# Kernel optimization log

Hardware: AMD Instinct MI355X
Metric: run time of the kernel (lower is better)

Reference implementation:

```python
import jax, jax.numpy as jnp
import numpy as np

# --- constants mirroring init_kwargs ---
DIM = 1024
N_HEADS = 16
N_KV_HEADS = 4
HEAD_DIM = DIM // N_HEADS          # 64
REP = N_HEADS // N_KV_HEADS        # 4
ROPE_THETA = 10000.0
WINDOW = 512
N_GLOBAL = 64
EPS = 1e-6


def setup_inputs() -> dict:
    key = jax.random.key(0)
    ks = jax.random.split(key, 7)
    B, L = 2, 2048
    x = jax.random.normal(ks[0], (B, L, DIM), dtype=jnp.float32)
    s = 0.02
    wq = jax.random.normal(ks[1], (DIM, N_HEADS * HEAD_DIM), dtype=jnp.float32) * s
    wk = jax.random.normal(ks[2], (DIM, N_KV_HEADS * HEAD_DIM), dtype=jnp.float32) * s
    wv = jax.random.normal(ks[3], (DIM, N_KV_HEADS * HEAD_DIM), dtype=jnp.float32) * s
    wo = jax.random.normal(ks[4], (N_HEADS * HEAD_DIM, DIM), dtype=jnp.float32) * s
    gq = jnp.ones((HEAD_DIM,), dtype=jnp.float32) + 0.01 * jax.random.normal(ks[5], (HEAD_DIM,), dtype=jnp.float32)
    gk = jnp.ones((HEAD_DIM,), dtype=jnp.float32) + 0.01 * jax.random.normal(ks[6], (HEAD_DIM,), dtype=jnp.float32)
    return {"x": x, "wq": wq, "wk": wk, "wv": wv, "wo": wo, "gq": gq, "gk": gk}


def _rmsnorm(t, g):
    # QKNorm: RMS norm over head_dim with learnable per-dim scale
    return t * jax.lax.rsqrt(jnp.mean(t * t, axis=-1, keepdims=True) + EPS) * g


def _rope(t, cos, sin):
    # t: [B,H,L,hd]; complex RoPE over consecutive pairs (2i, 2i+1)
    t1 = t[..., 0::2]
    t2 = t[..., 1::2]
    o1 = t1 * cos - t2 * sin
    o2 = t1 * sin + t2 * cos
    return jnp.stack([o1, o2], axis=-1).reshape(t.shape)


def reference(x, wq, wk, wv, wo, gq, gk):
    B, L, D = x.shape
    q = (x @ wq).reshape(B, L, N_HEADS, HEAD_DIM)
    k = (x @ wk).reshape(B, L, N_KV_HEADS, HEAD_DIM)
    v = (x @ wv).reshape(B, L, N_KV_HEADS, HEAD_DIM)
    q = _rmsnorm(q, gq)
    k = _rmsnorm(k, gk)
    q = q.transpose(0, 2, 1, 3)  # [B,H,L,hd]
    k = k.transpose(0, 2, 1, 3)
    v = v.transpose(0, 2, 1, 3)

    # RoPE frequencies (start_pos = 0)
    inv_freq = 1.0 / (ROPE_THETA ** (jnp.arange(0, HEAD_DIM, 2, dtype=jnp.float32) / HEAD_DIM))
    ang = jnp.arange(L, dtype=jnp.float32)[:, None] * inv_freq[None, :]  # [L, hd/2]
    cos, sin = jnp.cos(ang), jnp.sin(ang)
    q = _rope(q, cos, sin)
    k = _rope(k, cos, sin)

    # GQA: repeat kv heads (repeat_interleave on head dim)
    k = jnp.repeat(k, REP, axis=1)
    v = jnp.repeat(v, REP, axis=1)

    scores = jnp.einsum("bhqd,bhkd->bhqk", q, k) / np.sqrt(HEAD_DIM).astype(np.float32)

    # sliding-window + global-token causal mask
    half = WINDOW // 2
    i = jnp.arange(L)[:, None]
    j = jnp.arange(L)[None, :]
    m = (j <= i) & ((j >= i - half) | (j < N_GLOBAL))  # [L,L] bool
    scores = jnp.where(m[None, None], scores, -jnp.inf)

    attn = jax.nn.softmax(scores.astype(jnp.float32), axis=-1).astype(scores.dtype)
    out = jnp.einsum("bhqk,bhkd->bhqd", attn, v)
    out = out.transpose(0, 2, 1, 3).reshape(B, L, N_HEADS * HEAD_DIM)
    return out @ wo
```

## Files before the change

kernel.cpp:

```cpp
#include <hip/hip_runtime.h>
#include <hip/hip_bf16.h>

typedef __bf16 bf16x8 __attribute__((ext_vector_type(8)));
typedef __bf16 bf16x4 __attribute__((ext_vector_type(4)));
typedef float  f32x4  __attribute__((ext_vector_type(4)));
typedef short  s16x4  __attribute__((ext_vector_type(4)));

__device__ __forceinline__ __bf16 to_bf16(float f) {
    __hip_bfloat16 h = __float2bfloat16(f);
    return *reinterpret_cast<__bf16*>(&h);
}

__device__ __forceinline__ f32x4 mfma32(bf16x8 a, bf16x8 b, f32x4 c) {
    return __builtin_amdgcn_mfma_f32_16x16x32_bf16(a, b, c, 0, 0, 0);
}
__device__ __forceinline__ f32x4 mfma16(bf16x4 a, bf16x4 b, f32x4 c) {
#if __has_builtin(__builtin_amdgcn_mfma_f32_16x16x16_bf16)
    return __builtin_amdgcn_mfma_f32_16x16x16_bf16(a, b, c, 0, 0, 0);
#else
    return __builtin_amdgcn_mfma_f32_16x16x16bf16_1k(
        __builtin_bit_cast(s16x4, a), __builtin_bit_cast(s16x4, b), c, 0, 0, 0);
#endif
}

__device__ __forceinline__ void gload_lds16(const __bf16* g, __bf16* l) {
    __builtin_amdgcn_global_load_lds(
        (const __attribute__((address_space(1))) void*)g,
        (__attribute__((address_space(3))) void*)l, 16, 0, 0);
}


__global__ __launch_bounds__(256) void prep_k(const float* __restrict__ wq,
                                              const float* __restrict__ wk,
                                              const float* __restrict__ wv,
                                              const float* __restrict__ x,
                                              __bf16* __restrict__ WqkvT,
                                              __bf16* __restrict__ xb,
                                              float2* __restrict__ rope_tab) {
    int b = blockIdx.x, tid = threadIdx.x;
    if (b >= 3584) {
        int idx = (b - 3584) * 256 + tid;
        int pos = idx >> 5, f = idx & 31;
        float ex = (float)(2 * f) * (1.0f / 64.0f);
        float invf = expf(-ex * 9.210340371976184f);
        float ang = (float)pos * invf;
        rope_tab[idx] = make_float2(cosf(ang), sinf(ang));
        return;
    }
    if (b >= 1536) {
        int i = ((b - 1536) * 256 + tid) * 8;
        f32x4 a = *(const f32x4*)(x + i);
        f32x4 c = *(const f32x4*)(x + i + 4);
        bf16x8 h;
        h[0] = to_bf16(a.x); h[1] = to_bf16(a.y); h[2] = to_bf16(a.z); h[3] = to_bf16(a.w);
        h[4] = to_bf16(c.x); h[5] = to_bf16(c.y); h[6] = to_bf16(c.z); h[7] = to_bf16(c.w);
        *(bf16x8*)(xb + i) = h;
        return;
    }
    __shared__ float tile[32][33];
    const float* src; __bf16* dst; int N, idx;
    if (b < 1024)      { src = wq; dst = WqkvT;                        N = 1024; idx = b; }
    else if (b < 1280) { src = wk; dst = WqkvT + (size_t)1024 * 1024;  N = 256;  idx = b - 1024; }
    else               { src = wv; dst = WqkvT + (size_t)1280 * 1024;  N = 256;  idx = b - 1280; }
    int k0 = (idx & 31) * 32, n0 = (idx >> 5) * 32;
    int tx = tid & 31, ty = tid >> 5;
#pragma unroll
    for (int r = 0; r < 4; ++r) {
        int kk = ty + r * 8;
        tile[kk][tx] = src[(size_t)(k0 + kk) * N + n0 + tx];
    }
    __syncthreads();
#pragma unroll
    for (int r = 0; r < 4; ++r) {
        int nn = ty + r * 8;
        dst[(size_t)(n0 + nn) * 1024 + k0 + tx] = to_bf16(tile[tx][nn]);
    }
}

#define GEMM_CORE128(A, BT, K, M0, N0)                                          \
    __bf16* smem = (__bf16*)smem_raw;                                           \
    int tid = threadIdx.x;                                                      \
    int m0 = (M0), n0 = (N0);                                                   \
    int wid = tid >> 6, lane = tid & 63;                                        \
    int wm = (wid & 1) * 64, wn = (wid >> 1) * 32;                              \
    int lm = lane & 15, qd = lane >> 4;                                         \
    int srow = tid >> 2, sc4 = tid & 3;                                         \
    f32x4 acc[4][2] = {};                                                       \
    int nt = (K) / 64;                                                          \
    auto STAGE = [&](int bsel, int t) {                                         \
        __bf16* base = smem + bsel * 16384;                                     \
        _Pragma("unroll")                                                       \
        for (int kh = 0; kh < 2; ++kh)                                          \
            gload_lds16((A) + (size_t)(m0 + srow) * (K) + t * 64 + kh * 32 + sc4 * 8, \
                        base + kh * 4096 + wid * 512);                          \
        _Pragma("unroll")                                                       \
        for (int kh = 0; kh < 2; ++kh)                                          \
            gload_lds16((BT) + (size_t)(n0 + srow) * (K) + t * 64 + kh * 32 + sc4 * 8, \
                        base + 8192 + kh * 4096 + wid * 512);                   \
    };                                                                          \
    STAGE(0, 0);                                                                \
    for (int t = 0; t < nt; ++t) {                                              \
        if (t + 1 < nt) {                                                       \
            STAGE((t + 1) & 1, t + 1);                                          \
            asm volatile("s_waitcnt vmcnt(4)" ::: "memory");                    \
        } else {                                                                \
            asm volatile("s_waitcnt vmcnt(0)" ::: "memory");                    \
        }                                                                       \
        __builtin_amdgcn_s_barrier();                                           \
        __builtin_amdgcn_sched_barrier(0);                                      \
        const __bf16* cA = smem + (t & 1) * 16384;                              \
        const __bf16* cB = cA + 8192;                                           \
        _Pragma("unroll")                                                       \
        for (int kh = 0; kh < 2; ++kh) {                                        \
            bf16x8 af[4], bfr[2];                                               \
            _Pragma("unroll")                                                   \
            for (int t4 = 0; t4 < 4; ++t4) {                                    \
                int row = wm + t4 * 16 + lm;                                    \
                af[t4] = *(const bf16x8*)&cA[kh * 4096 + row * 32 + qd * 8];    \
            }                                                                   \
            _Pragma("unroll")                                                   \
            for (int j = 0; j < 2; ++j) {                                       \
                int col = wn + j * 16 + lm;                                     \
                bfr[j] = *(const bf16x8*)&cB[kh * 4096 + col * 32 + qd * 8];    \
            }                                                                   \
            _Pragma("unroll")                                                   \
            for (int ti = 0; ti < 4; ++ti)                                      \
                _Pragma("unroll")                                               \
                for (int tj = 0; tj < 2; ++tj)                                  \
                    acc[ti][tj] = mfma32(af[ti], bfr[tj], acc[ti][tj]);         \
        }                                                                       \
        asm volatile("s_waitcnt lgkmcnt(0)" ::: "memory");                      \
        __builtin_amdgcn_s_barrier();                                           \
    }

__global__ __launch_bounds__(512) void gemmqkv_k(const __bf16* __restrict__ A,
                                                 const __bf16* __restrict__ BT,
                                                 const float2* __restrict__ rope_tab,
                                                 const float* __restrict__ gq,
                                                 const float* __restrict__ gk,
                                                 const float* __restrict__ wo,
                                                 __bf16* __restrict__ Qb,
                                                 __bf16* __restrict__ Kbl,
                                                 __bf16* __restrict__ Vt,
                                                 __bf16* __restrict__ WoT) {
    extern __shared__ char smem_raw[];
    if (blockIdx.y >= 12) {
        float* scr = (float*)smem_raw;
        int bidT = (blockIdx.y - 12) * 32 + blockIdx.x;
        int sub = threadIdx.x >> 8, t8 = threadIdx.x & 255;
        int tx = t8 & 31, ty = t8 >> 5;
        float* my = scr + sub * 1056;
#pragma unroll
        for (int r = 0; r < 4; ++r) {
            int tile = bidT * 8 + r * 2 + sub;
            int k0 = (tile & 31) * 32, n0t = (tile >> 5) * 32;
            __syncthreads();
#pragma unroll
            for (int rr = 0; rr < 4; ++rr) {
                int kk = ty + rr * 8;
                my[kk * 33 + tx] = wo[(size_t)(k0 + kk) * 1024 + n0t + tx];
            }
            __syncthreads();
#pragma unroll
            for (int rr = 0; rr < 4; ++rr) {
                int nn = ty + rr * 8;
                WoT[(size_t)(n0t + nn) * 1024 + k0 + tx] = to_bf16(my[tx * 33 + nn]);
            }
        }
        return;
    }
    __shared__ float ssp[4][128];
    int gidb = blockIdx.y * 32 + blockIdx.x;
    int swzb = (gidb & 7) * 48 + (gidb >> 3);
    GEMM_CORE128(A, BT, 1024, (swzb & 31) * 128, (swzb >> 5) * 128)
    int head0 = n0 >> 6;
    int quad = wid >> 1;
    int chead = wn & 63;

    if (head0 < 20) {
        int head = head0 + (quad >> 1);
        bool isq = head < 16;
        const float* gvec = isq ? gq : gk;
        float gam[2];
#pragma unroll
        for (int tj = 0; tj < 2; ++tj) gam[tj] = gvec[chead + tj * 16 + lm];

#pragma unroll
        for (int ti = 0; ti < 4; ++ti)
#pragma unroll
            for (int r = 0; r < 4; ++r) {
                float sq = acc[ti][0][r] * acc[ti][0][r] + acc[ti][1][r] * acc[ti][1][r];
                sq += __shfl_xor(sq, 1);
                sq += __shfl_xor(sq, 2);
                sq += __shfl_xor(sq, 4);
                sq += __shfl_xor(sq, 8);
                if (lm == 0) ssp[quad][wm + ti * 16 + qd * 4 + r] = sq;
            }
        __syncthreads();

#pragma unroll
        for (int ti = 0; ti < 4; ++ti)
#pragma unroll
            for (int r = 0; r < 4; ++r) {
                int row = wm + ti * 16 + qd * 4 + r;
                int t = m0 + row;
                int pos = t & 2047, bb = t >> 11;
                float ss = ssp[quad][row] + ssp[quad ^ 1][row];
                float scale = rsqrtf(ss * (1.0f / 64.0f) + 1e-6f);
#pragma unroll
                for (int tj = 0; tj < 2; ++tj) {
                    int cw = chead + tj * 16 + lm;
                    float v = acc[ti][tj][r] * scale * gam[tj];
                    float2 cs = rope_tab[pos * 32 + (cw >> 1)];
                    float pv = __shfl_xor(v, 1);
                    float outv = (cw & 1) ? (pv * cs.y + v * cs.x) : (v * cs.x - pv * cs.y);
                    if (isq) {
                        int kvh = head >> 2, h4 = head & 3;
                        size_t off = (((((size_t)bb * 4 + kvh) * 128 + (pos >> 4)) * 4 + h4) * 16
                                      + (pos & 15)) * 64 + cw;
                        Qb[off] = to_bf16(outv * 0.125f);
                    } else {
                        int kvg = head - 16;
                        Kbl[(((size_t)bb * 4 + kvg) * 2048 + pos) * 64 + cw] = to_bf16(outv);
                    }
                }
            }
    } else {
        __bf16* tvh = smem + (quad >> 1) * 8704;
        int bb = m0 >> 11, pos0 = m0 & 2047;
#pragma unroll
        for (int ti = 0; ti < 4; ++ti)
#pragma unroll
            for (int tj = 0; tj < 2; ++tj)
#pragma unroll
                for (int r = 0; r < 4; ++r) {
                    int row = wm + ti * 16 + qd * 4 + r;
                    int cw = chead + tj * 16 + lm;
                    tvh[cw * 136 + row] = to_bf16(acc[ti][tj][r]);
                }
        __syncthreads();
        int hh = tid >> 8, t8 = tid & 255;
        int kvg = head0 + hh - 20;
        size_t gg = (size_t)bb * 4 + kvg;
        const __bf16* tvr = smem + hh * 8704;
#pragma unroll
        for (int p = 0; p < 4; ++p) {
            int d = p * 16 + (t8 >> 4);
            int tok = (t8 & 15) * 8;
            bf16x8 vvv = *(const bf16x8*)&tvr[d * 136 + tok];
            *(bf16x8*)(Vt + (gg * 64 + d) * 2048 + pos0 + tok) = vvv;
        }
    }
}

__global__ __launch_bounds__(512) void gemm_bf16_k(const __bf16* __restrict__ A,
                                                   const __bf16* __restrict__ BT,
                                                   float* __restrict__ C,
                                                   int K, int N) {
    extern __shared__ char smem_raw[];
    int gidb = blockIdx.y * 32 + blockIdx.x;
    int swzb = (gidb & 7) * 32 + (gidb >> 3);
    GEMM_CORE128(A, BT, K, (swzb & 31) * 128, (swzb >> 5) * 128)
#pragma unroll
    for (int ti = 0; ti < 4; ++ti)
#pragma unroll
        for (int tj = 0; tj < 2; ++tj)
#pragma unroll
            for (int r = 0; r < 4; ++r) {
                int row = m0 + wm + ti * 16 + qd * 4 + r;
                int col = n0 + wn + tj * 16 + lm;
                C[(size_t)row * N + col] = acc[ti][tj][r];
            }
}

__global__ __launch_bounds__(512) void attn_k(const __bf16* __restrict__ Qb,
                                              const __bf16* __restrict__ Kbl,
                                              const __bf16* __restrict__ Vt,
                                              __bf16* __restrict__ aout) {
    __shared__ __bf16 Kt[2][64 * 64];
    __shared__ __bf16 Vl[2][64 * 64];
    int tid = threadIdx.x, wid = tid >> 6, lane = tid & 63;
    int l15 = lane & 15, quad = lane >> 4;
    int qb = blockIdx.x, kvh = blockIdx.y, b = blockIdx.z;
    int qg = wid >> 2;
    int h4 = wid & 3;
    int iw0 = qb * 32;
    int iw = iw0 + qg * 16;
    int g = b * 4 + kvh;
    int h = kvh * 4 + h4;
    int e7 = l15 & 7;

    int qbi = qb * 2 + qg;
    const __bf16* qp = Qb + ((((size_t)g * 128 + qbi) * 4 + h4) * 16 + l15) * 64 + quad * 8;
    bf16x8 qf0 = *(const bf16x8*)qp;
    bf16x8 qf1 = *(const bf16x8*)(qp + 32);

    int ts = (iw0 - 256) >> 6; if (ts < 1) ts = 1;
    int tmaxb = (iw0 + 31) >> 6;
    int n_all = (tmaxb >= ts) ? (tmaxb - ts + 2) : 1;
    int tmaxw = (iw + 15) >> 6;

    const __bf16* Kg = Kbl + (size_t)g * 2048 * 64;
    const __bf16* Vg = Vt + (size_t)g * 64 * 2048;

    int r0 = tid >> 3, c0 = tid & 7;
    int kl = r0 * 64 + ((c0 ^ (r0 & 7)) * 8);

    bf16x8 kr, vr;
    auto stage_load = [&](int tt) {
        kr = *(const bf16x8*)(Kg + (size_t)tt * 64 * 64 + r0 * 64 + c0 * 8);
        vr = *(const bf16x8*)(Vg + (size_t)r0 * 2048 + tt * 64 + c0 * 8);
    };
    auto stage_write = [&](int buf) {
        *(bf16x8*)&Kt[buf][kl] = kr;
        *(bf16x8*)&Vl[buf][kl] = vr;
    };

    stage_load(0);
    stage_write(0);

    f32x4 o[4] = {};
    float mr = -1e30f, lrp = 0.f;
    int iq = iw + l15;

    for (int idx = 0; idx < n_all; ++idx) {
        int tt = (idx == 0) ? 0 : ts + idx - 1;
        if (idx + 1 < n_all) stage_load(ts + idx);
        __syncthreads();
        int buf = idx & 1;

        f32x4 s[4] = {};
#pragma unroll
        for (int nt = 0; nt < 4; ++nt) {
            const __bf16* kp = &Kt[buf][(nt * 16 + l15) * 64];
            bf16x8 k0 = *(const bf16x8*)(kp + ((quad ^ e7) * 8));
            bf16x8 k1 = *(const bf16x8*)(kp + (((quad + 4) ^ e7) * 8));
            s[nt] = mfma32(k0, qf0, s[nt]);
            s[nt] = mfma32(k1, qf1, s[nt]);
        }

        bool need_mask = (tt >= tmaxw) || (tt >= 1 && tt * 64 < iw + 15 - 256);
        if (need_mask) {
#pragma unroll
            for (int nt = 0; nt < 4; ++nt)
#pragma unroll
                for (int r = 0; r < 4; ++r) {
                    int j = tt * 64 + nt * 16 + quad * 4 + r;
                    bool valid = (j <= iq) && ((j >= iq - 256) || (j < 64));
                    s[nt][r] = valid ? s[nt][r] : -1e30f;
                }
        }

        float mx = -1e30f;
#pragma unroll
        for (int nt = 0; nt < 4; ++nt)
#pragma unroll
            for (int r = 0; r < 4; ++r) mx = fmaxf(mx, s[nt][r]);
        mx = fmaxf(mx, __shfl_xor(mx, 16));
        mx = fmaxf(mx, __shfl_xor(mx, 32));
        float mn = fmaxf(mr, mx);
        float alpha = __expf(mr - mn);
        mr = mn;

        float ps = 0.f;
        bf16x4 pb[4];
#pragma unroll
        for (int nt = 0; nt < 4; ++nt)
#pragma unroll
            for (int r = 0; r < 4; ++r) {
                float pv = __expf(s[nt][r] - mn);
                ps += pv;
                pb[nt][r] = to_bf16(pv);
            }
        lrp = lrp * alpha + ps;

#pragma unroll
        for (int dt = 0; dt < 4; ++dt) {
            o[dt] *= alpha;
            const __bf16* vp = &Vl[buf][(dt * 16 + l15) * 64];
#pragma unroll
            for (int nt = 0; nt < 4; ++nt) {
                int c8 = 2 * nt + (quad >> 1);
                bf16x4 va = *(const bf16x4*)(vp + ((c8 ^ e7) * 8) + (quad & 1) * 4);
                o[dt] = mfma16(va, pb[nt], o[dt]);
            }
        }

        if (idx + 1 < n_all) stage_write((idx + 1) & 1);
    }

    lrp += __shfl_xor(lrp, 16);
    lrp += __shfl_xor(lrp, 32);
    float inv = 1.f / lrp;
    __syncthreads();
    __bf16* pr = (__bf16*)Kt + wid * 16 * 64;
#pragma unroll
    for (int dt = 0; dt < 4; ++dt)
#pragma unroll
        for (int r = 0; r < 4; ++r) {
            int e = dt * 16 + quad * 4 + r;
            int c8 = e >> 3;
            pr[l15 * 64 + ((c8 ^ e7) * 8) + (e & 7)] = to_bf16(o[dt][r] * inv);
        }
    bf16x8 o0 = *(const bf16x8*)(pr + l15 * 64 + (((2 * quad) ^ e7) * 8));
    bf16x8 o1 = *(const bf16x8*)(pr + l15 * 64 + (((2 * quad + 1) ^ e7) * 8));
    __bf16* op = aout + ((size_t)b * 2048 + iw + l15) * 1024 + h * 64 + quad * 16;
    *(bf16x8*)op = o0;
    *(bf16x8*)(op + 8) = o1;
}

extern "C" void kernel_launch(void* const* d_in, const int* in_sizes, int n_in,
                              void* d_out, int out_size, void* d_ws, size_t ws_size,
                              hipStream_t stream) {
    const float* x  = (const float*)d_in[0];
    const float* wq = (const float*)d_in[1];
    const float* wk = (const float*)d_in[2];
    const float* wv = (const float*)d_in[3];
    const float* wo = (const float*)d_in[4];
    const float* gq = (const float*)d_in[5];
    const float* gk = (const float*)d_in[6];
    float* out = (float*)d_out;

    char* ws = (char*)d_ws;
    __bf16*  WqkvT = (__bf16*)ws;
    __bf16*  WoT   = (__bf16*)(ws + 3145728);
    __bf16*  xb_ao = (__bf16*)(ws + 5242880);
    __bf16*  Kbl   = (__bf16*)(ws + 13631488);
    __bf16*  Vt    = (__bf16*)(ws + 15728640);
    __bf16*  Qb    = (__bf16*)(ws + 17825792);
    float2*  rtab  = (float2*)(ws + 26214400);

    prep_k<<<3840, dim3(256), 0, stream>>>(wq, wk, wv, x, WqkvT, xb_ao, rtab);
    gemmqkv_k<<<dim3(32, 16), dim3(512), 65536, stream>>>(xb_ao, WqkvT, rtab, gq, gk, wo,
                                                          Qb, Kbl, Vt, WoT);
    attn_k<<<dim3(64, 4, 2), dim3(512), 0, stream>>>(Qb, Kbl, Vt, xb_ao);
    gemm_bf16_k<<<dim3(32, 8), dim3(512), 65536, stream>>>(xb_ao, WoT, out, 1024, 1024);
}
```

Baseline: 143.7 us.

## Use smaller tiles for output projection, vectorize transposes, add occupancy hints

The output projection GEMM now uses a dedicated 128x64 tile kernel, which doubles the grid to 512 blocks for better CU coverage at the cost of lower per-block reuse. The fp32-to-bf16 weight transposes switch to float4 loads and 4-wide bf16 stores with a padded LDS tile. The grid swizzle in the QKV GEMM is removed in favour of direct block mapping. Launch bounds with a minimum of 4 blocks per CU are added to constrain register use, which may cause spills.

```diff
diff --git a/kernel.cpp b/kernel.cpp
--- a/kernel.cpp
+++ b/kernel.cpp
@@ -57,24 +57,19 @@
         *(bf16x8*)(xb + i) = h;
         return;
     }
-    __shared__ float tile[32][33];
+    __shared__ float tile[32][36];
     const float* src; __bf16* dst; int N, idx;
     if (b < 1024)      { src = wq; dst = WqkvT;                        N = 1024; idx = b; }
     else if (b < 1280) { src = wk; dst = WqkvT + (size_t)1024 * 1024;  N = 256;  idx = b - 1024; }
     else               { src = wv; dst = WqkvT + (size_t)1280 * 1024;  N = 256;  idx = b - 1280; }
     int k0 = (idx & 31) * 32, n0 = (idx >> 5) * 32;
-    int tx = tid & 31, ty = tid >> 5;
-#pragma unroll
-    for (int r = 0; r < 4; ++r) {
-        int kk = ty + r * 8;
-        tile[kk][tx] = src[(size_t)(k0 + kk) * N + n0 + tx];
-    }
+    int row = tid >> 3, c4 = tid & 7;
+    *(f32x4*)&tile[row][c4 * 4] = *(const f32x4*)(src + (size_t)(k0 + row) * N + n0 + c4 * 4);
     __syncthreads();
-#pragma unroll
-    for (int r = 0; r < 4; ++r) {
-        int nn = ty + r * 8;
-        dst[(size_t)(n0 + nn) * 1024 + k0 + tx] = to_bf16(tile[tx][nn]);
-    }
+    bf16x4 v;
+#pragma unroll
+    for (int j = 0; j < 4; ++j) v[j] = to_bf16(tile[c4 * 4 + j][row]);
+    *(bf16x4*)&dst[(size_t)(n0 + row) * 1024 + k0 + c4 * 4] = v;
 }
 
 #define GEMM_CORE128(A, BT, K, M0, N0)                                          \
@@ -133,46 +128,40 @@
         __builtin_amdgcn_s_barrier();                                           \
     }
 
-__global__ __launch_bounds__(512) void gemmqkv_k(const __bf16* __restrict__ A,
-                                                 const __bf16* __restrict__ BT,
-                                                 const float2* __restrict__ rope_tab,
-                                                 const float* __restrict__ gq,
-                                                 const float* __restrict__ gk,
-                                                 const float* __restrict__ wo,
-                                                 __bf16* __restrict__ Qb,
-                                                 __bf16* __restrict__ Kbl,
-                                                 __bf16* __restrict__ Vt,
-                                                 __bf16* __restrict__ WoT) {
+__global__ __launch_bounds__(512, 4) void gemmqkv_k(const __bf16* __restrict__ A,
+                                                    const __bf16* __restrict__ BT,
+                                                    const float2* __restrict__ rope_tab,
+                                                    const float* __restrict__ gq,
+                                                    const float* __restrict__ gk,
+                                                    const float* __restrict__ wo,
+                                                    __bf16* __restrict__ Qb,
+                                                    __bf16* __restrict__ Kbl,
+                                                    __bf16* __restrict__ Vt,
+                                                    __bf16* __restrict__ WoT) {
     extern __shared__ char smem_raw[];
     if (blockIdx.y >= 12) {
         float* scr = (float*)smem_raw;
         int bidT = (blockIdx.y - 12) * 32 + blockIdx.x;
         int sub = threadIdx.x >> 8, t8 = threadIdx.x & 255;
-        int tx = t8 & 31, ty = t8 >> 5;
-        float* my = scr + sub * 1056;
+        int row = t8 >> 3, c4 = t8 & 7;
+        float* my = scr + sub * 1152;
 #pragma unroll
         for (int r = 0; r < 4; ++r) {
             int tile = bidT * 8 + r * 2 + sub;
             int k0 = (tile & 31) * 32, n0t = (tile >> 5) * 32;
             __syncthreads();
-#pragma unroll
-            for (int rr = 0; rr < 4; ++rr) {
-                int kk = ty + rr * 8;
-                my[kk * 33 + tx] = wo[(size_t)(k0 + kk) * 1024 + n0t + tx];
-            }
+            *(f32x4*)&my[row * 36 + c4 * 4] =
+                *(const f32x4*)(wo + (size_t)(k0 + row) * 1024 + n0t + c4 * 4);
             __syncthreads();
-#pragma unroll
-            for (int rr = 0; rr < 4; ++rr) {
-                int nn = ty + rr * 8;
-                WoT[(size_t)(n0t + nn) * 1024 + k0 + tx] = to_bf16(my[tx * 33 + nn]);
-            }
+            bf16x4 v;
+#pragma unroll
+            for (int j = 0; j < 4; ++j) v[j] = to_bf16(my[(c4 * 4 + j) * 36 + row]);
+            *(bf16x4*)&WoT[(size_t)(n0t + row) * 1024 + k0 + c4 * 4] = v;
         }
         return;
     }
     __shared__ float ssp[4][128];
-    int gidb = blockIdx.y * 32 + blockIdx.x;
-    int swzb = (gidb & 7) * 48 + (gidb >> 3);
-    GEMM_CORE128(A, BT, 1024, (swzb & 31) * 128, (swzb >> 5) * 128)
+    GEMM_CORE128(A, BT, 1024, blockIdx.x * 128, blockIdx.y * 128)
     int head0 = n0 >> 6;
     int quad = wid >> 1;
     int chead = wn & 63;
@@ -253,30 +242,76 @@
     }
 }
 
-__global__ __launch_bounds__(512) void gemm_bf16_k(const __bf16* __restrict__ A,
-                                                   const __bf16* __restrict__ BT,
-                                                   float* __restrict__ C,
-                                                   int K, int N) {
+__global__ __launch_bounds__(512, 4) void gemm_op_k(const __bf16* __restrict__ A,
+                                                    const __bf16* __restrict__ BT,
+                                                    float* __restrict__ C) {
     extern __shared__ char smem_raw[];
-    int gidb = blockIdx.y * 32 + blockIdx.x;
-    int swzb = (gidb & 7) * 32 + (gidb >> 3);
-    GEMM_CORE128(A, BT, K, (swzb & 31) * 128, (swzb >> 5) * 128)
-#pragma unroll
-    for (int ti = 0; ti < 4; ++ti)
+    __bf16* smem = (__bf16*)smem_raw;
+    int tid = threadIdx.x;
+    int m0 = blockIdx.x * 128, n0 = blockIdx.y * 64;
+    int wid = tid >> 6, lane = tid & 63;
+    int wm = (wid & 3) * 32, wn = (wid >> 2) * 32;
+    int lm = lane & 15, qd = lane >> 4;
+    int srow = tid >> 2, sc4 = tid & 3;
+    int bhalf = wid >> 2, bidx = tid & 255;
+    int brow = bidx >> 2, bc4 = bidx & 3;
+    f32x4 acc[2][2] = {};
+    auto STAGE = [&](int bsel, int t) {
+        __bf16* base = smem + bsel * 12288;
+#pragma unroll
+        for (int kh = 0; kh < 2; ++kh)
+            gload_lds16(A + (size_t)(m0 + srow) * 1024 + t * 64 + kh * 32 + sc4 * 8,
+                        base + kh * 4096 + wid * 512);
+        gload_lds16(BT + (size_t)(n0 + brow) * 1024 + t * 64 + bhalf * 32 + bc4 * 8,
+                    base + 8192 + bhalf * 2048 + (wid & 3) * 512);
+    };
+    STAGE(0, 0);
+    for (int t = 0; t < 16; ++t) {
+        if (t + 1 < 16) {
+            STAGE((t + 1) & 1, t + 1);
+            asm volatile("s_waitcnt vmcnt(3)" ::: "memory");
+        } else {
+            asm volatile("s_waitcnt vmcnt(0)" ::: "memory");
+        }
+        __builtin_amdgcn_s_barrier();
+        __builtin_amdgcn_sched_barrier(0);
+        const __bf16* cA = smem + (t & 1) * 12288;
+        const __bf16* cB = cA + 8192;
+#pragma unroll
+        for (int kh = 0; kh < 2; ++kh) {
+            bf16x8 af[2], bfr[2];
+#pragma unroll
+            for (int i = 0; i < 2; ++i) {
+                int row = wm + i * 16 + lm;
+                af[i] = *(const bf16x8*)&cA[kh * 4096 + row * 32 + qd * 8];
+                int col = wn + i * 16 + lm;
+                bfr[i] = *(const bf16x8*)&cB[kh * 2048 + col * 32 + qd * 8];
+            }
+#pragma unroll
+            for (int ti = 0; ti < 2; ++ti)
+#pragma unroll
+                for (int tj = 0; tj < 2; ++tj)
+                    acc[ti][tj] = mfma32(af[ti], bfr[tj], acc[ti][tj]);
+        }
+        asm volatile("s_waitcnt lgkmcnt(0)" ::: "memory");
+        __builtin_amdgcn_s_barrier();
+    }
+#pragma unroll
+    for (int ti = 0; ti < 2; ++ti)
 #pragma unroll
         for (int tj = 0; tj < 2; ++tj)
 #pragma unroll
             for (int r = 0; r < 4; ++r) {
                 int row = m0 + wm + ti * 16 + qd * 4 + r;
                 int col = n0 + wn + tj * 16 + lm;
-                C[(size_t)row * N + col] = acc[ti][tj][r];
-            }
-}
-
-__global__ __launch_bounds__(512) void attn_k(const __bf16* __restrict__ Qb,
-                                              const __bf16* __restrict__ Kbl,
-                                              const __bf16* __restrict__ Vt,
-                                              __bf16* __restrict__ aout) {
+                C[(size_t)row * 1024 + col] = acc[ti][tj][r];
+            }
+}
+
+__global__ __launch_bounds__(512, 4) void attn_k(const __bf16* __restrict__ Qb,
+                                                 const __bf16* __restrict__ Kbl,
+                                                 const __bf16* __restrict__ Vt,
+                                                 __bf16* __restrict__ aout) {
     __shared__ __bf16 Kt[2][64 * 64];
     __shared__ __bf16 Vl[2][64 * 64];
     int tid = threadIdx.x, wid = tid >> 6, lane = tid & 63;
@@ -434,5 +469,5 @@
     gemmqkv_k<<<dim3(32, 16), dim3(512), 65536, stream>>>(xb_ao, WqkvT, rtab, gq, gk, wo,
                                                           Qb, Kbl, Vt, WoT);
     attn_k<<<dim3(64, 4, 2), dim3(512), 0, stream>>>(Qb, Kbl, Vt, xb_ao);
-    gemm_bf16_k<<<dim3(32, 8), dim3(512), 65536, stream>>>(xb_ao, WoT, out, 1024, 1024);
-}
+    gemm_op_k<<<dim3(32, 16), dim3(512), 49152, stream>>>(xb_ao, WoT, out);
+}
```

Measured after the change: 143.4 us. No clear change (-0.2%).
